# Kernel optimization log

Hardware: AMD Instinct MI355X
Metric: run time of the kernel (lower is better)

## Reference

```python
import jax, jax.numpy as jnp
import numpy as np

DIM = 1024
NUM_HEADS = 16
HEAD_DIM = DIM // NUM_HEADS
SCALE = HEAD_DIM ** -0.5


def setup_inputs() -> dict:
    key = jax.random.key(0)
    ks = jax.random.split(key, 6)
    B, N = 2, 2048
    s = DIM ** -0.5
    return {
        "x": jax.random.normal(ks[0], (B, N, DIM), dtype=jnp.float32),
        "Wq": jax.random.normal(ks[1], (DIM, DIM), dtype=jnp.float32) * s,
        "Wk": jax.random.normal(ks[2], (DIM, DIM), dtype=jnp.float32) * s,
        "Wv": jax.random.normal(ks[3], (DIM, DIM), dtype=jnp.float32) * s,
        "Wp": jax.random.normal(ks[4], (DIM, DIM), dtype=jnp.float32) * s,
        "bp": jax.random.normal(ks[5], (DIM,), dtype=jnp.float32) * 0.01,
    }


def reference(x, Wq, Wk, Wv, Wp, bp):
    B, N, C = x.shape
    H, D = NUM_HEADS, HEAD_DIM
    # projections (torch Linear: x @ W.T); reshape to (B, H, N, D)
    q = (x @ Wq.T).reshape(B, N, H, D).transpose(0, 2, 1, 3)
    k = (x @ Wk.T).reshape(B, N, H, D).transpose(0, 2, 1, 3)
    v = (x @ Wv.T).reshape(B, N, H, D).transpose(0, 2, 1, 3)
    attn = jnp.einsum("bhnd,bhmd->bhnm", q, k) * SCALE
    attn = jax.nn.softmax(attn, axis=-1)  # dropout p=0 -> identity
    out = jnp.einsum("bhnm,bhmd->bhnd", attn, v)
    out = out.transpose(0, 2, 1, 3).reshape(B, N, C)
    return out @ Wp.T + bp
```

## Files before the change

### kernel.cpp

```cpp
#include <hip/hip_runtime.h>
#include <cstdint>

#define DIMC   1024
#define NHEADS 16
#define HD     64
#define BATCH  2
#define SEQ    2048
#define MROWS  (BATCH*SEQ)
#define QSCALE2 0.18033688f

typedef __bf16 bf16x8 __attribute__((ext_vector_type(8)));
typedef float  f32x4  __attribute__((ext_vector_type(4)));

#define TST 136

__device__ __forceinline__ unsigned short f2bf(float f) {
    union { float f; unsigned int u; } v; v.f = f;
    unsigned int u = v.u;
    u += 0x7fffu + ((u >> 16) & 1u);
    return (unsigned short)(u >> 16);
}

__device__ __forceinline__ unsigned int pk2bf(float a, float b) {
    union { float f; unsigned int u; } ua, ub;
    ua.f = a; ub.f = b;
    return __builtin_amdgcn_perm(ub.u + 0x8000u, ua.u + 0x8000u, 0x07060302u);
}

__device__ __forceinline__ void gload_lds16(const void* g, void* l) {
    __builtin_amdgcn_global_load_lds(
        (const __attribute__((address_space(1))) unsigned int*)g,
        (__attribute__((address_space(3))) unsigned int*)l, 16, 0, 0);
}

__global__ __launch_bounds__(256) void cast_all(
    const float* __restrict__ x,
    const float* __restrict__ Wq, const float* __restrict__ Wk,
    const float* __restrict__ Wv, const float* __restrict__ Wp,
    unsigned short* __restrict__ xb, unsigned short* __restrict__ Wb)
{
    const size_t M1 = (size_t)DIMC * DIMC;
    int y = blockIdx.y;
    const float* src;
    unsigned short* dst;
    if (y < 4)      { src = x  + (size_t)y * M1; dst = xb + (size_t)y * M1; }
    else if (y == 4){ src = Wq; dst = Wb; }
    else if (y == 5){ src = Wk; dst = Wb + M1; }
    else if (y == 6){ src = Wv; dst = Wb + 2 * M1; }
    else            { src = Wp; dst = Wb + 3 * M1; }
    size_t idx = ((size_t)blockIdx.x * 256 + threadIdx.x) * 4;
    float4 v = *(const float4*)(src + idx);
    ushort4 p; p.x = f2bf(v.x); p.y = f2bf(v.y); p.z = f2bf(v.z); p.w = f2bf(v.w);
    *(ushort4*)(dst + idx) = p;
}

__device__ __forceinline__ void gemm_issue32(
    const unsigned short* __restrict__ A, const unsigned short* __restrict__ B,
    unsigned short* As, unsigned short* Bs, int m0, int n0, int kt)
{
    const int t = threadIdx.x;
    const int rr = t >> 2, cg = t & 3;
#pragma unroll
    for (int i = 0; i < 2; ++i) {
        int r  = i * 64 + rr;
        int sc = cg ^ ((r >> 1) & 3);
        int dst = (r >> 1) * 64 + (r & 1) * 32 + cg * 8;
        gload_lds16(A + (size_t)(m0 + r) * DIMC + kt + sc * 8, As + dst);
        gload_lds16(B + (size_t)(n0 + r) * DIMC + kt + sc * 8, Bs + dst);
    }
}

__device__ __forceinline__ void gemm_compute32(
    const unsigned short* As, const unsigned short* Bs, f32x4 acc[4][4])
{
    const int t = threadIdx.x;
    const int w = t >> 6, lane = t & 63, quad = lane >> 4, lr = lane & 15;
    const int wr = w >> 1, wc = w & 1;
    bf16x8 af[4], bfr[4];
#pragma unroll
    for (int mt = 0; mt < 4; ++mt) {
        int row = wr * 64 + mt * 16 + lr;
        af[mt] = *(const bf16x8*)&As[(row >> 1) * 64 + (row & 1) * 32
                                     + ((quad ^ ((row >> 1) & 3)) * 8)];
    }
#pragma unroll
    for (int nt = 0; nt < 4; ++nt) {
        int row = wc * 64 + nt * 16 + lr;
        bfr[nt] = *(const bf16x8*)&Bs[(row >> 1) * 64 + (row & 1) * 32
                                      + ((quad ^ ((row >> 1) & 3)) * 8)];
    }
#pragma unroll
    for (int mt = 0; mt < 4; ++mt)
#pragma unroll
        for (int nt = 0; nt < 4; ++nt)
            acc[mt][nt] = __builtin_amdgcn_mfma_f32_16x16x32_bf16(af[mt], bfr[nt], acc[mt][nt], 0, 0, 0);
}

__device__ __forceinline__ void gemm_k_loop_db32(
    const unsigned short* __restrict__ A, const unsigned short* __restrict__ B,
    unsigned short* smem, int m0, int n0, f32x4 acc[4][4])
{
    unsigned short* As0 = smem;
    unsigned short* Bs0 = smem + 4096;
    unsigned short* As1 = smem + 8192;
    unsigned short* Bs1 = smem + 12288;

    gemm_issue32(A, B, As0, Bs0, m0, n0, 0);
    for (int kt = 0; kt < DIMC; kt += 64) {
        __syncthreads();
        gemm_issue32(A, B, As1, Bs1, m0, n0, kt + 32);
        gemm_compute32(As0, Bs0, acc);
        __syncthreads();
        if (kt + 64 < DIMC) gemm_issue32(A, B, As0, Bs0, m0, n0, kt + 64);
        gemm_compute32(As1, Bs1, acc);
    }
}

__device__ __forceinline__ void vt_epilogue(
    unsigned short* Ts, f32x4 acc[4][4], int m0, int n0,
    unsigned short* __restrict__ vT)
{
    const int t = threadIdx.x;
    const int w = t >> 6, lane = t & 63, quad = lane >> 4, lr = lane & 15;
    const int wr = w >> 1, wc = w & 1;

    __syncthreads();
#pragma unroll
    for (int mt = 0; mt < 4; ++mt)
#pragma unroll
        for (int nt = 0; nt < 4; ++nt) {
            int lcol  = wc * 64 + nt * 16 + lr;
            int lrow0 = wr * 64 + mt * 16 + quad * 4;
            ushort4 p;
            p.x = f2bf(acc[mt][nt][0]); p.y = f2bf(acc[mt][nt][1]);
            p.z = f2bf(acc[mt][nt][2]); p.w = f2bf(acc[mt][nt][3]);
            *(ushort4*)&Ts[lcol * TST + lrow0] = p;
        }
    __syncthreads();

    int lc = t >> 1, half = t & 1;
    int cg = n0 + lc, hh = cg >> 6, dd = cg & 63;
    int bb = m0 >> 11, nn0 = m0 & (SEQ - 1);
    size_t dst = ((size_t)((bb * NHEADS + hh) * HD + dd)) * SEQ + nn0 + half * 64;
    const unsigned short* srcp = &Ts[lc * TST + half * 64];
#pragma unroll
    for (int i = 0; i < 8; ++i)
        *(uint4*)&vT[dst + i * 8] = *(const uint4*)&srcp[i * 8];
}

__global__ __launch_bounds__(256, 3) void gemm_qkv_fast(
    const unsigned short* __restrict__ xb, const unsigned short* __restrict__ Wb,
    unsigned short* __restrict__ qo, unsigned short* __restrict__ ko,
    unsigned short* __restrict__ vT)
{
    __shared__ unsigned short smem[17408];

    const int t  = threadIdx.x;
    const int lin = blockIdx.y * 8 + blockIdx.x;
    const int T   = (lin & 7) * 32 + (lin >> 3);
    const int n0 = (T & 7) * 128, m0 = (T >> 3) * 128, z = blockIdx.z;
    const unsigned short* B = Wb + (size_t)z * DIMC * DIMC;
    const int w = t >> 6, lane = t & 63, quad = lane >> 4, lr = lane & 15;
    const int wr = w >> 1, wc = w & 1;

    f32x4 acc[4][4];
#pragma unroll
    for (int mt = 0; mt < 4; ++mt)
#pragma unroll
        for (int nt = 0; nt < 4; ++nt)
#pragma unroll
            for (int r = 0; r < 4; ++r) acc[mt][nt][r] = 0.f;

    gemm_k_loop_db32(xb, B, smem, m0, n0, acc);

    if (z == 2) {
        vt_epilogue(smem, acc, m0, n0, vT);
    } else {
        unsigned short* Out = (z == 0) ? qo : ko;
        const float sc = (z == 0) ? QSCALE2 : 1.0f;
#pragma unroll
        for (int mt = 0; mt < 4; ++mt)
#pragma unroll
            for (int nt = 0; nt < 4; ++nt)
#pragma unroll
                for (int r = 0; r < 4; ++r) {
                    int row = m0 + wr * 64 + mt * 16 + quad * 4 + r;
                    int col = n0 + wc * 64 + nt * 16 + lr;
                    Out[(size_t)row * DIMC + col] = f2bf(acc[mt][nt][r] * sc);
                }
    }
}

__device__ __forceinline__ void gemm_issue_out(
    const unsigned short* __restrict__ A, const unsigned short* __restrict__ B,
    unsigned short* As, unsigned short* Bs, int m0, int n0, int kt)
{
    const int t = threadIdx.x;
    const int w = t >> 6, lane = t & 63;
    const int srow = lane >> 3, scol = lane & 7;
#pragma unroll
    for (int i = 0; i < 4; ++i) {
        int r  = i * 32 + w * 8 + srow;
        int cg = scol ^ (r & 7);
        gload_lds16(A + (size_t)(m0 + r) * DIMC + kt + cg * 8, As + r * 64 + scol * 8);
    }
#pragma unroll
    for (int i = 0; i < 2; ++i) {
        int r  = i * 32 + w * 8 + srow;
        int cg = scol ^ (r & 7);
        gload_lds16(B + (size_t)(n0 + r) * DIMC + kt + cg * 8, Bs + r * 64 + scol * 8);
    }
}

__device__ __forceinline__ void gemm_compute_out(
    const unsigned short* As, const unsigned short* Bs, f32x4 acc[4][2])
{
    const int t = threadIdx.x;
    const int w = t >> 6, lane = t & 63, quad = lane >> 4, lr = lane & 15;
    const int wr = w >> 1, wc = w & 1;
#pragma unroll
    for (int kk = 0; kk < 2; ++kk) {
        bf16x8 af[4], bfr[2];
#pragma unroll
        for (int mt = 0; mt < 4; ++mt) {
            int row = wr * 64 + mt * 16 + lr;
            int cb  = kk * 4 + quad;
            af[mt] = *(const bf16x8*)&As[row * 64 + (cb ^ (row & 7)) * 8];
        }
#pragma unroll
        for (int nt = 0; nt < 2; ++nt) {
            int row = wc * 32 + nt * 16 + lr;
            int cb  = kk * 4 + quad;
            bfr[nt] = *(const bf16x8*)&Bs[row * 64 + (cb ^ (row & 7)) * 8];
        }
#pragma unroll
        for (int mt = 0; mt < 4; ++mt)
#pragma unroll
            for (int nt = 0; nt < 2; ++nt)
                acc[mt][nt] = __builtin_amdgcn_mfma_f32_16x16x32_bf16(af[mt], bfr[nt], acc[mt][nt], 0, 0, 0);
    }
}

__global__ __launch_bounds__(256, 3) void gemm_out_fast(
    const unsigned short* __restrict__ O, const unsigned short* __restrict__ Wpb,
    const float* __restrict__ bias, float* __restrict__ out)
{
    __shared__ unsigned short smem[24576];

    const int t  = threadIdx.x;
    const int lin = blockIdx.y * 16 + blockIdx.x;
    const int T   = (lin & 7) * 64 + (lin >> 3);
    const int n0 = (T & 15) * 64, m0 = (T >> 4) * 128;
    const int w = t >> 6, lane = t & 63, quad = lane >> 4, lr = lane & 15;
    const int wr = w >> 1, wc = w & 1;

    f32x4 acc[4][2];
#pragma unroll
    for (int mt = 0; mt < 4; ++mt)
#pragma unroll
        for (int nt = 0; nt < 2; ++nt)
#pragma unroll
            for (int r = 0; r < 4; ++r) acc[mt][nt][r] = 0.f;

    unsigned short* As0 = smem;
    unsigned short* Bs0 = smem + 8192;
    unsigned short* As1 = smem + 12288;
    unsigned short* Bs1 = smem + 20480;

    gemm_issue_out(O, Wpb, As0, Bs0, m0, n0, 0);
    for (int kt = 0; kt < DIMC; kt += 128) {
        __syncthreads();
        gemm_issue_out(O, Wpb, As1, Bs1, m0, n0, kt + 64);
        gemm_compute_out(As0, Bs0, acc);
        __syncthreads();
        if (kt + 128 < DIMC) gemm_issue_out(O, Wpb, As0, Bs0, m0, n0, kt + 128);
        gemm_compute_out(As1, Bs1, acc);
    }

#pragma unroll
    for (int mt = 0; mt < 4; ++mt)
#pragma unroll
        for (int nt = 0; nt < 2; ++nt)
#pragma unroll
            for (int r = 0; r < 4; ++r) {
                int row = m0 + wr * 64 + mt * 16 + quad * 4 + r;
                int col = n0 + wc * 32 + nt * 16 + lr;
                out[(size_t)row * DIMC + col] = acc[mt][nt][r] + bias[col];
            }
}

__global__ __launch_bounds__(256, 2) void attn_kernel(
    const unsigned short* __restrict__ qg, const unsigned short* __restrict__ kg,
    const unsigned short* __restrict__ vT, unsigned short* __restrict__ og)
{
    __shared__ unsigned short Ka[64 * 64];
    __shared__ unsigned short Kb[64 * 64];
    __shared__ unsigned short Va[64 * 64];
    __shared__ unsigned short Vb[64 * 64];
    __shared__ unsigned short PsA[128 * 64];
    __shared__ unsigned short PsB[128 * 64];

    const int t  = threadIdx.x;
    const int w = t >> 6, l = t & 63, quad = l >> 4, lr = l & 15;
    const int srow = t >> 3, scol = t & 7;
    const int pkey = (lr & 7) << 1;

    const int bid  = blockIdx.x;
    const int slot = bid >> 3;
    const int bh   = (bid & 7) * 4 + (slot >> 4);
    const int qt   = slot & 15;
    const int b    = bh >> 4, h = bh & 15;

    const unsigned short* khead = kg + ((size_t)(b * SEQ)) * DIMC + h * HD;
    const unsigned short* vhead = vT + (size_t)((b * NHEADS + h) * HD) * SEQ;

    bf16x8 qf[2][2];
#pragma unroll
    for (int mt = 0; mt < 2; ++mt) {
        const size_t qoff = ((size_t)(b * SEQ + qt * 128 + w * 32 + mt * 16 + lr)) * DIMC + h * HD;
        qf[mt][0] = *(const bf16x8*)(qg + qoff + 0  + quad * 8);
        qf[mt][1] = *(const bf16x8*)(qg + qoff + 32 + quad * 8);
    }

    bf16x8 ones;
#pragma unroll
    for (int j = 0; j < 8; ++j) ones[j] = (__bf16)1.0f;
    const f32x4 fzero = { 0.f, 0.f, 0.f, 0.f };

    f32x4 o_acc[2][4], lacc[2];
#pragma unroll
    for (int mt = 0; mt < 2; ++mt) {
        lacc[mt] = fzero;
#pragma unroll
        for (int ct = 0; ct < 4; ++ct) o_acc[mt][ct] = fzero;
    }

    auto issue = [&](int kt, unsigned short* Kd, unsigned short* Vd) {
#pragma unroll
        for (int i = 0; i < 2; ++i) {
            int r  = i * 32 + srow;
            int cg = scol ^ (r & 7);
            gload_lds16(khead + (size_t)(kt * 64 + r) * DIMC + cg * 8, Kd + r * 64 + scol * 8);
            gload_lds16(vhead + (size_t)r * SEQ + kt * 64 + cg * 8,   Vd + r * 64 + scol * 8);
        }
    };

    auto s_phase = [&](const unsigned short* Kc, f32x4 (&s)[2][4]) {
        __builtin_amdgcn_s_setprio(1);
#pragma unroll
        for (int nt = 0; nt < 4; ++nt) {
            int row = nt * 16 + lr;
            bf16x8 kf = *(const bf16x8*)&Kc[row * 64 + ((quad ^ (row & 7)) * 8)];
#pragma unroll
            for (int mt = 0; mt < 2; ++mt)
                s[mt][nt] = __builtin_amdgcn_mfma_f32_16x16x32_bf16(kf, qf[mt][0], fzero, 0, 0, 0);
        }
#pragma unroll
        for (int nt = 0; nt < 4; ++nt) {
            int row = nt * 16 + lr;
            bf16x8 kf = *(const bf16x8*)&Kc[row * 64 + (((4 + quad) ^ (row & 7)) * 8)];
#pragma unroll
            for (int mt = 0; mt < 2; ++mt)
                s[mt][nt] = __builtin_amdgcn_mfma_f32_16x16x32_bf16(kf, qf[mt][1], s[mt][nt], 0, 0, 0);
        }
        __builtin_amdgcn_s_setprio(0);
    };

    auto exp_store = [&](const f32x4 (&s)[2][4], unsigned short* PsW) {
#pragma unroll
        for (int mt = 0; mt < 2; ++mt)
#pragma unroll
            for (int nt = 0; nt < 4; ++nt) {
                uint2 pp;
                pp.x = pk2bf(__builtin_amdgcn_exp2f(s[mt][nt][0]),
                             __builtin_amdgcn_exp2f(s[mt][nt][1]));
                pp.y = pk2bf(__builtin_amdgcn_exp2f(s[mt][nt][2]),
                             __builtin_amdgcn_exp2f(s[mt][nt][3]));
                *(uint2*)&PsW[(w * 32 + mt * 16 + lr) * 64 + (((nt * 4 + quad) ^ pkey) * 4)] = pp;
            }
    };

    auto vload = [&](const unsigned short* Vc, bf16x8 (&vr)[8]) {
#pragma unroll
        for (int kk = 0; kk < 2; ++kk)
#pragma unroll
            for (int ct = 0; ct < 4; ++ct) {
                int row = ct * 16 + lr;
                vr[kk * 4 + ct] = *(const bf16x8*)&Vc[row * 64 + (((kk * 4 + quad) ^ (row & 7)) * 8)];
            }
    };

    auto pv = [&](const unsigned short* PsR, const bf16x8 (&vr)[8]) {
        __builtin_amdgcn_s_setprio(1);
#pragma unroll
        for (int kk = 0; kk < 2; ++kk)
#pragma unroll
            for (int mt = 0; mt < 2; ++mt) {
                bf16x8 pf = *(const bf16x8*)&PsR[(w * 32 + mt * 16 + lr) * 64 + (((kk * 8 + quad * 2) ^ pkey) * 4)];
                lacc[mt] = __builtin_amdgcn_mfma_f32_16x16x32_bf16(pf, ones, lacc[mt], 0, 0, 0);
#pragma unroll
                for (int ct = 0; ct < 4; ++ct)
                    o_acc[mt][ct] = __builtin_amdgcn_mfma_f32_16x16x32_bf16(pf, vr[kk * 4 + ct], o_acc[mt][ct], 0, 0, 0);
            }
        __builtin_amdgcn_s_setprio(0);
    };

    bf16x8 vrA[8], vrB[8];

    issue(0, Ka, Va);
    for (int kt = 0; kt < SEQ / 64; kt += 2) {
        __syncthreads();
        issue(kt + 1, Kb, Vb);
        {
            f32x4 s[2][4];
            s_phase(Ka, s);
            if (kt) pv(PsB, vrB);
            exp_store(s, PsA);
            vload(Va, vrA);
        }
        __syncthreads();
        if (kt + 2 < SEQ / 64) issue(kt + 2, Ka, Va);
        {
            f32x4 s[2][4];
            s_phase(Kb, s);
            pv(PsA, vrA);
            exp_store(s, PsB);
            vload(Vb, vrB);
        }
    }
    pv(PsB, vrB);

#pragma unroll
    for (int mt = 0; mt < 2; ++mt) {
        float inv[4];
#pragma unroll
        for (int r = 0; r < 4; ++r) inv[r] = 1.0f / lacc[mt][r];
#pragma unroll
        for (int ct = 0; ct < 4; ++ct)
#pragma unroll
            for (int r = 0; r < 4; ++r) {
                int qrow = qt * 128 + w * 32 + mt * 16 + quad * 4 + r;
                og[((size_t)(b * SEQ + qrow)) * DIMC + h * HD + ct * 16 + lr] =
                    f2bf(o_acc[mt][ct][r] * inv[r]);
            }
    }
}

extern "C" void kernel_launch(void* const* d_in, const int* in_sizes, int n_in,
                              void* d_out, int out_size, void* d_ws, size_t ws_size,
                              hipStream_t stream)
{
    (void)in_sizes; (void)n_in; (void)out_size; (void)ws_size;

    const float* x  = (const float*)d_in[0];
    const float* Wq = (const float*)d_in[1];
    const float* Wk = (const float*)d_in[2];
    const float* Wv = (const float*)d_in[3];
    const float* Wp = (const float*)d_in[4];
    const float* bp = (const float*)d_in[5];
    float* out = (float*)d_out;

    const size_t SZ  = (size_t)MROWS * DIMC;
    const size_t WSZ = (size_t)DIMC * DIMC;

    unsigned short* q  = (unsigned short*)d_ws;
    unsigned short* k  = q + SZ;
    unsigned short* vt = k + SZ;
    unsigned short* o  = vt + SZ;
    unsigned short* Wb = o + SZ;
    unsigned short* xb = o;

    cast_all<<<dim3(1024, 8), 256, 0, stream>>>(x, Wq, Wk, Wv, Wp, xb, Wb);
    gemm_qkv_fast<<<dim3(8, 32, 3), 256, 0, stream>>>(xb, Wb, q, k, vt);
    attn_kernel<<<dim3(512), 256, 0, stream>>>(q, k, vt, o);
    gemm_out_fast<<<dim3(16, 32), 256, 0, stream>>>(o, Wb + 3 * WSZ, bp, out);
}
```

Before: 172.0 us.

## Triple-buffer QKV GEMM and attention loads with partial vmcnt waits

Both the QKV projection GEMM and the attention kernel move from double-buffered LDS tiles with full __syncthreads to a three-stage ring of buffers. Each stage waits only on the older outstanding global-to-LDS loads (s_waitcnt vmcnt(4)) before a raw barrier, so two tiles stay in flight during compute. Attention also drops the second P buffer and V register set, since each wave reads and writes only its own P rows. The cost is more GEMM shared memory (about 48KB per block), which could reduce occupancy. Correctness depends on each issue call emitting exactly four loads per thread.

```diff
diff --git a/kernel.cpp b/kernel.cpp
--- a/kernel.cpp
+++ b/kernel.cpp
@@ -32,6 +32,13 @@
         (const __attribute__((address_space(1))) unsigned int*)g,
         (__attribute__((address_space(3))) unsigned int*)l, 16, 0, 0);
 }
+
+#define WAITBAR4() do { asm volatile("s_waitcnt vmcnt(4)" ::: "memory"); \
+                        __builtin_amdgcn_s_barrier();                    \
+                        __builtin_amdgcn_sched_barrier(0); } while (0)
+#define WAITBAR0() do { asm volatile("s_waitcnt vmcnt(0)" ::: "memory"); \
+                        __builtin_amdgcn_s_barrier();                    \
+                        __builtin_amdgcn_sched_barrier(0); } while (0)
 
 __global__ __launch_bounds__(256) void cast_all(
     const float* __restrict__ x,
@@ -96,26 +103,6 @@
             acc[mt][nt] = __builtin_amdgcn_mfma_f32_16x16x32_bf16(af[mt], bfr[nt], acc[mt][nt], 0, 0, 0);
 }
 
-__device__ __forceinline__ void gemm_k_loop_db32(
-    const unsigned short* __restrict__ A, const unsigned short* __restrict__ B,
-    unsigned short* smem, int m0, int n0, f32x4 acc[4][4])
-{
-    unsigned short* As0 = smem;
-    unsigned short* Bs0 = smem + 4096;
-    unsigned short* As1 = smem + 8192;
-    unsigned short* Bs1 = smem + 12288;
-
-    gemm_issue32(A, B, As0, Bs0, m0, n0, 0);
-    for (int kt = 0; kt < DIMC; kt += 64) {
-        __syncthreads();
-        gemm_issue32(A, B, As1, Bs1, m0, n0, kt + 32);
-        gemm_compute32(As0, Bs0, acc);
-        __syncthreads();
-        if (kt + 64 < DIMC) gemm_issue32(A, B, As0, Bs0, m0, n0, kt + 64);
-        gemm_compute32(As1, Bs1, acc);
-    }
-}
-
 __device__ __forceinline__ void vt_epilogue(
     unsigned short* Ts, f32x4 acc[4][4], int m0, int n0,
     unsigned short* __restrict__ vT)
@@ -153,7 +140,13 @@
     unsigned short* __restrict__ qo, unsigned short* __restrict__ ko,
     unsigned short* __restrict__ vT)
 {
-    __shared__ unsigned short smem[17408];
+    __shared__ unsigned short smem[24576];
+    unsigned short* As0 = smem;
+    unsigned short* Bs0 = smem + 4096;
+    unsigned short* As1 = smem + 8192;
+    unsigned short* Bs1 = smem + 12288;
+    unsigned short* As2 = smem + 16384;
+    unsigned short* Bs2 = smem + 20480;
 
     const int t  = threadIdx.x;
     const int lin = blockIdx.y * 8 + blockIdx.x;
@@ -171,7 +164,19 @@
 #pragma unroll
             for (int r = 0; r < 4; ++r) acc[mt][nt][r] = 0.f;
 
-    gemm_k_loop_db32(xb, B, smem, m0, n0, acc);
+    gemm_issue32(xb, B, As0, Bs0, m0, n0, 0);
+    gemm_issue32(xb, B, As1, Bs1, m0, n0, 32);
+
+    for (int base = 0; base < 30; base += 3) {
+        WAITBAR4(); gemm_issue32(xb, B, As2, Bs2, m0, n0, (base + 2) * 32);
+        gemm_compute32(As0, Bs0, acc);
+        WAITBAR4(); gemm_issue32(xb, B, As0, Bs0, m0, n0, (base + 3) * 32);
+        gemm_compute32(As1, Bs1, acc);
+        WAITBAR4(); gemm_issue32(xb, B, As1, Bs1, m0, n0, (base + 4) * 32);
+        gemm_compute32(As2, Bs2, acc);
+    }
+    WAITBAR4(); gemm_compute32(As0, Bs0, acc);
+    WAITBAR0(); gemm_compute32(As1, Bs1, acc);
 
     if (z == 2) {
         vt_epilogue(smem, acc, m0, n0, vT);
@@ -293,12 +298,13 @@
     const unsigned short* __restrict__ qg, const unsigned short* __restrict__ kg,
     const unsigned short* __restrict__ vT, unsigned short* __restrict__ og)
 {
-    __shared__ unsigned short Ka[64 * 64];
-    __shared__ unsigned short Kb[64 * 64];
-    __shared__ unsigned short Va[64 * 64];
-    __shared__ unsigned short Vb[64 * 64];
-    __shared__ unsigned short PsA[128 * 64];
-    __shared__ unsigned short PsB[128 * 64];
+    __shared__ unsigned short K0s[64 * 64];
+    __shared__ unsigned short K1s[64 * 64];
+    __shared__ unsigned short K2s[64 * 64];
+    __shared__ unsigned short V0s[64 * 64];
+    __shared__ unsigned short V1s[64 * 64];
+    __shared__ unsigned short V2s[64 * 64];
+    __shared__ unsigned short Ps[128 * 64];
 
     const int t  = threadIdx.x;
     const int w = t >> 6, l = t & 63, quad = l >> 4, lr = l & 15;
@@ -366,7 +372,7 @@
         __builtin_amdgcn_s_setprio(0);
     };
 
-    auto exp_store = [&](const f32x4 (&s)[2][4], unsigned short* PsW) {
+    auto exp_store = [&](const f32x4 (&s)[2][4]) {
 #pragma unroll
         for (int mt = 0; mt < 2; ++mt)
 #pragma unroll
@@ -376,11 +382,12 @@
                              __builtin_amdgcn_exp2f(s[mt][nt][1]));
                 pp.y = pk2bf(__builtin_amdgcn_exp2f(s[mt][nt][2]),
                              __builtin_amdgcn_exp2f(s[mt][nt][3]));
-                *(uint2*)&PsW[(w * 32 + mt * 16 + lr) * 64 + (((nt * 4 + quad) ^ pkey) * 4)] = pp;
+                *(uint2*)&Ps[(w * 32 + mt * 16 + lr) * 64 + (((nt * 4 + quad) ^ pkey) * 4)] = pp;
             }
     };
 
-    auto vload = [&](const unsigned short* Vc, bf16x8 (&vr)[8]) {
+    bf16x8 vr[8];
+    auto vload = [&](const unsigned short* Vc) {
 #pragma unroll
         for (int kk = 0; kk < 2; ++kk)
 #pragma unroll
@@ -390,13 +397,13 @@
             }
     };
 
-    auto pv = [&](const unsigned short* PsR, const bf16x8 (&vr)[8]) {
+    auto pv = [&]() {
         __builtin_amdgcn_s_setprio(1);
 #pragma unroll
         for (int kk = 0; kk < 2; ++kk)
 #pragma unroll
             for (int mt = 0; mt < 2; ++mt) {
-                bf16x8 pf = *(const bf16x8*)&PsR[(w * 32 + mt * 16 + lr) * 64 + (((kk * 8 + quad * 2) ^ pkey) * 4)];
+                bf16x8 pf = *(const bf16x8*)&Ps[(w * 32 + mt * 16 + lr) * 64 + (((kk * 8 + quad * 2) ^ pkey) * 4)];
                 lacc[mt] = __builtin_amdgcn_mfma_f32_16x16x32_bf16(pf, ones, lacc[mt], 0, 0, 0);
 #pragma unroll
                 for (int ct = 0; ct < 4; ++ct)
@@ -405,30 +412,25 @@
         __builtin_amdgcn_s_setprio(0);
     };
 
-    bf16x8 vrA[8], vrB[8];
-
-    issue(0, Ka, Va);
-    for (int kt = 0; kt < SEQ / 64; kt += 2) {
-        __syncthreads();
-        issue(kt + 1, Kb, Vb);
-        {
-            f32x4 s[2][4];
-            s_phase(Ka, s);
-            if (kt) pv(PsB, vrB);
-            exp_store(s, PsA);
-            vload(Va, vrA);
-        }
-        __syncthreads();
-        if (kt + 2 < SEQ / 64) issue(kt + 2, Ka, Va);
-        {
-            f32x4 s[2][4];
-            s_phase(Kb, s);
-            pv(PsA, vrA);
-            exp_store(s, PsB);
-            vload(Vb, vrB);
-        }
-    }
-    pv(PsB, vrB);
+    auto subphase = [&](const unsigned short* Kc, const unsigned short* Vc, bool first) {
+        f32x4 s[2][4];
+        s_phase(Kc, s);
+        if (!first) pv();
+        exp_store(s);
+        vload(Vc);
+    };
+
+    issue(0, K0s, V0s);
+    issue(1, K1s, V1s);
+
+    for (int base = 0; base < 30; base += 3) {
+        WAITBAR4(); issue(base + 2, K2s, V2s); subphase(K0s, V0s, base == 0);
+        WAITBAR4(); issue(base + 3, K0s, V0s); subphase(K1s, V1s, false);
+        WAITBAR4(); issue(base + 4, K1s, V1s); subphase(K2s, V2s, false);
+    }
+    WAITBAR4(); subphase(K0s, V0s, false);
+    WAITBAR0(); subphase(K1s, V1s, false);
+    pv();
 
 #pragma unroll
     for (int mt = 0; mt < 2; ++mt) {
```

Result: no change. 173.2 us (+0.7%).
